# Optimization experiments

Hardware: AMD Instinct MI355X
Metric: run time of the kernel (lower is better)

The kernel has to match this reference:

```python
import jax, jax.numpy as jnp
import numpy as np

N = 4096
TAU = 0.2          # args.tau relaxation temperature
EPS = 1e-10        # numerical guard for logit of clamped probs


def setup_inputs() -> dict:
    key = jax.random.key(0)
    k1, k2, k3 = jax.random.split(key, 3)
    r = jax.random.uniform(k1, (N, N))
    ori_adj = jnp.where(r < 0.005, -1.0, jnp.where(r < 0.01, 1.0, 0.0)).astype(jnp.float32)
    # nn.init.uniform_(change_links_prob, 0.0, 0.001)
    change_links_prob = jax.random.uniform(k2, (N, N), minval=0.0, maxval=0.001, dtype=jnp.float32)
    # uniform noise for the RelaxedBernoulli logistic reparameterization
    u = jax.random.uniform(k3, (N, N), minval=1e-6, maxval=1.0 - 1e-6, dtype=jnp.float32)
    return {"ori_adj": ori_adj, "change_links_prob": change_links_prob, "u": u}


def reference(ori_adj, change_links_prob, u):
    # --- get_modified_adj: RelaxedBernoulliStraightThrough(tau, clamp(p,0,1)).rsample() ---
    p = jnp.clip(change_links_prob, EPS, 1.0 - EPS)      # torch.clamp(p, 0, 1) + logit guard
    logits = jnp.log(p) - jnp.log1p(-p)
    noise = jnp.log(u) - jnp.log1p(-u)                   # logistic noise
    soft = jax.nn.sigmoid((logits + noise) / TAU)        # relaxed sample
    hard = jnp.round(soft)                               # quantized sample
    change_prob = soft + jax.lax.stop_gradient(hard - soft)  # straight-through
    mod_adj = ori_adj + change_prob * (-2.0 * ori_adj)   # ori_adj * (1 - 2*b)

    # --- balance_degree_directed(mod_adj) ---
    # torch.diag(matrix) returns the diagonal VECTOR, broadcast-subtracted per row (faithful).
    A = mod_adj + mod_adj.T - jnp.diag(mod_adj)
    A_abs = jnp.abs(A)
    tr3 = jnp.einsum('ij,jk,ki->', A, A, A)              # trace(A @ A @ A)
    tr3_abs = jnp.einsum('ij,jk,ki->', A_abs, A_abs, A_abs)
    balance = 0.5 * (1.0 + tr3 / tr3_abs)
    return mod_adj, balance
```

## Files before the change

### kernel.cpp

```cpp
#include <hip/hip_runtime.h>
#include <hip/hip_bf16.h>
#include <cstdint>
#include <cstddef>

#define N 4096
#define NN ((size_t)N * (size_t)N)

typedef int   int4v   __attribute__((ext_vector_type(4)));
typedef float float4v __attribute__((ext_vector_type(4)));

__device__ inline void async16(const void* g, void* lds) {
    __builtin_amdgcn_global_load_lds(
        (const __attribute__((address_space(1))) void*)g,
        (__attribute__((address_space(3))) void*)lds, 16, 0, 0);
}

__global__ __launch_bounds__(256) void fused_mod_build(
        const float* __restrict__ ori,
        const float* __restrict__ clp,
        const float* __restrict__ uu,
        float* __restrict__ out,
        signed char* __restrict__ A,
        signed char* __restrict__ AT,
        signed char* __restrict__ Aa,
        signed char* __restrict__ ATa,
        double* __restrict__ accs) {
    const int I = blockIdx.x, J = blockIdx.y;
    if (I > J) return;
    __shared__ float sm1[64][65];
    __shared__ float sm2[64][65];
    __shared__ float dI[64], dJ[64];
    const int t = threadIdx.x;
    const int r = t >> 2;
    const int q = t & 3;
    const int bi = I * 64, bj = J * 64;
    if (I == 0 && J == 0 && t < 2) accs[t] = 0.0;
    if (t < 128) {
        const int x = (t < 64) ? (bi + t) : (bj + (t - 64));
        const size_t off = (size_t)x * N + x;
        const float o = ori[off];
        const float hard = (clp[off] + uu[off] >= 1.0f) ? 1.0f : 0.0f;
        const float d = fmaf(hard, -2.0f * o, o);
        if (t < 64) dI[t] = d; else dJ[t - 64] = d;
    }
    #pragma unroll
    for (int k = 0; k < 4; ++k) {
        const size_t off = (size_t)(bi + r) * N + bj + k * 16 + q * 4;
        const float4v o4 = *(const float4v*)(ori + off);
        const float4v p4 = *(const float4v*)(clp + off);
        const float4v u4 = *(const float4v*)(uu + off);
        float4v m;
        #pragma unroll
        for (int c = 0; c < 4; ++c) {
            const float hard = (p4[c] + u4[c] >= 1.0f) ? 1.0f : 0.0f;
            m[c] = fmaf(hard, -2.0f * o4[c], o4[c]);
            sm1[r][k * 16 + q * 4 + c] = m[c];
        }
        *(float4v*)(out + off) = m;
    }
    #pragma unroll
    for (int k = 0; k < 4; ++k) {
        const size_t off = (size_t)(bj + r) * N + bi + k * 16 + q * 4;
        const float4v o4 = *(const float4v*)(ori + off);
        const float4v p4 = *(const float4v*)(clp + off);
        const float4v u4 = *(const float4v*)(uu + off);
        float4v m;
        #pragma unroll
        for (int c = 0; c < 4; ++c) {
            const float hard = (p4[c] + u4[c] >= 1.0f) ? 1.0f : 0.0f;
            m[c] = fmaf(hard, -2.0f * o4[c], o4[c]);
            sm2[r][k * 16 + q * 4 + c] = m[c];
        }
        if (I != J) *(float4v*)(out + off) = m;
    }
    __syncthreads();
    int pkA1[4], pkAa1[4], pkT1[4], pkTa1[4];
    int pkA2[4], pkAa2[4], pkT2[4], pkTa2[4];
    #pragma unroll
    for (int w = 0; w < 4; ++w) {
        int a1w = 0, aa1w = 0, t1w = 0, ta1w = 0;
        int a2w = 0, aa2w = 0, t2w = 0, ta2w = 0;
        #pragma unroll
        for (int k = 0; k < 4; ++k) {
            const int c = q * 16 + w * 4 + k;
            const float a1 = sm1[r][c] + sm2[c][r] - dJ[c];
            const int v1 = (int)a1;  const int u1 = v1 < 0 ? -v1 : v1;
            a1w  |= (v1 & 255) << (8 * k);
            aa1w |= (u1 & 255) << (8 * k);
            const float t1 = sm1[c][r] + sm2[r][c] - dJ[r];
            const int w1 = (int)t1;  const int x1 = w1 < 0 ? -w1 : w1;
            t1w  |= (w1 & 255) << (8 * k);
            ta1w |= (x1 & 255) << (8 * k);
            const float a2 = sm2[r][c] + sm1[c][r] - dI[c];
            const int v2 = (int)a2;  const int u2 = v2 < 0 ? -v2 : v2;
            a2w  |= (v2 & 255) << (8 * k);
            aa2w |= (u2 & 255) << (8 * k);
            const float t2 = sm2[c][r] + sm1[r][c] - dI[r];
            const int w2 = (int)t2;  const int x2 = w2 < 0 ? -w2 : w2;
            t2w  |= (w2 & 255) << (8 * k);
            ta2w |= (x2 & 255) << (8 * k);
        }
        pkA1[w] = a1w; pkAa1[w] = aa1w; pkT1[w] = t1w; pkTa1[w] = ta1w;
        pkA2[w] = a2w; pkAa2[w] = aa2w; pkT2[w] = t2w; pkTa2[w] = ta2w;
    }
    const size_t oIJ = (size_t)(bi + r) * N + bj + q * 16;
    const size_t oJI = (size_t)(bj + r) * N + bi + q * 16;
    *(int4v*)&A  [oIJ] = *(int4v*)pkA1;
    *(int4v*)&Aa [oIJ] = *(int4v*)pkAa1;
    *(int4v*)&AT [oJI] = *(int4v*)pkT1;
    *(int4v*)&ATa[oJI] = *(int4v*)pkTa1;
    if (I != J) {
        *(int4v*)&A  [oJI] = *(int4v*)pkA2;
        *(int4v*)&Aa [oJI] = *(int4v*)pkAa2;
        *(int4v*)&AT [oIJ] = *(int4v*)pkT2;
        *(int4v*)&ATa[oIJ] = *(int4v*)pkTa2;
    }
}

#define BK 64
#define NT (N / BK)
#define BUFSZ 32768

__global__ __launch_bounds__(512, 2) void gemm_trace_i8(
        const signed char* __restrict__ Ag,
        const signed char* __restrict__ ATg,
        const signed char* __restrict__ Aag,
        const signed char* __restrict__ ATag,
        double* __restrict__ accs) {
    __shared__ __align__(16) signed char lds[4 * BUFSZ];
    __shared__ int red[8];
    const int z = blockIdx.z;
    const signed char* Asrc = z ? Aag  : Ag;
    const signed char* Bsrc = z ? ATag : ATg;
    const int i0 = blockIdx.y * 256;
    const int k0 = blockIdx.x * 256;
    const int t = threadIdx.x;
    const int lane = t & 63;
    const int wave = t >> 6;
    const int wm = wave >> 2;
    const int wn = wave & 3;
    const int quad = lane >> 4;
    const int col  = lane & 15;

    const int c1 = t;
    const int r1 = c1 >> 2;
    const int r2 = r1 + 128;
    const int s1 = (((c1 & 3) ^ ((r1 >> 1) & 3)) << 4);
    const int s2 = (((c1 & 3) ^ ((r2 >> 1) & 3)) << 4);
    const signed char* gA1 = Asrc + (size_t)(i0 + r1) * N + s1;
    const signed char* gA2 = Asrc + (size_t)(i0 + r2) * N + s2;
    const signed char* gB1 = Bsrc + (size_t)(k0 + r1) * N + s1;
    const signed char* gB2 = Bsrc + (size_t)(k0 + r2) * N + s2;
    const int ldsA1 = (wave * 64) * 16;
    const int ldsA2 = 8192  + (wave * 64) * 16;
    const int ldsB1 = 16384 + (wave * 64) * 16;
    const int ldsB2 = 24576 + (wave * 64) * 16;
    const int fsw = ((quad ^ ((col >> 1) & 3)) << 4);

    int4v acc[8][4];
    #pragma unroll
    for (int a = 0; a < 8; ++a)
        #pragma unroll
        for (int b = 0; b < 4; ++b)
            acc[a][b] = (int4v){0, 0, 0, 0};

    for (int p = 0; p < 3; ++p) {
        const int pb = p * BUFSZ;
        const size_t go = (size_t)p * BK;
        async16(gA1 + go, lds + pb + ldsA1);
        async16(gA2 + go, lds + pb + ldsA2);
        async16(gB1 + go, lds + pb + ldsB1);
        async16(gB2 + go, lds + pb + ldsB2);
    }
    asm volatile("s_waitcnt vmcnt(8)" ::: "memory");
    __builtin_amdgcn_s_barrier();
    __builtin_amdgcn_sched_barrier(0);

    for (int j = 0; j < NT; ++j) {
        const int buf = (j & 3) * BUFSZ;
        const signed char* Ab = lds + buf;
        const signed char* Bb = lds + buf + 16384;
        const int pre = j + 3;
        const size_t go = (size_t)pre * BK;
        const int pb = (pre & 3) * BUFSZ;
        int4v af0[4], af1[4], bf[4];
        af0[0] = *(const int4v*)(Ab + ((wm * 128 + 0 * 16 + col) << 6) + fsw);
        #pragma unroll
        for (int tc = 0; tc < 4; ++tc)
            bf[tc] = *(const int4v*)(Bb + ((wn * 64 + tc * 16 + col) << 6) + fsw);
        #pragma unroll
        for (int tr = 1; tr < 4; ++tr)
            af0[tr] = *(const int4v*)(Ab + ((wm * 128 + tr * 16 + col) << 6) + fsw);
        #pragma unroll
        for (int tr = 0; tr < 4; ++tr)
            af1[tr] = *(const int4v*)(Ab + ((wm * 128 + 64 + tr * 16 + col) << 6) + fsw);
        if (pre < NT) {
            async16(gA1 + go, lds + pb + ldsA1);
            async16(gA2 + go, lds + pb + ldsA2);
            async16(gB1 + go, lds + pb + ldsB1);
            async16(gB2 + go, lds + pb + ldsB2);
        }
        __builtin_amdgcn_s_setprio(1);
        asm volatile("s_waitcnt lgkmcnt(7)" ::: "memory");
        __builtin_amdgcn_sched_barrier(0);
        #pragma unroll
        for (int tc = 0; tc < 4; ++tc)
            acc[0][tc] = __builtin_amdgcn_mfma_i32_16x16x64_i8(af0[0], bf[tc], acc[0][tc], 0, 0, 0);
        #pragma unroll
        for (int tr = 1; tr < 4; ++tr) {
            if (tr == 1)      asm volatile("s_waitcnt lgkmcnt(6)" ::: "memory");
            else if (tr == 2) asm volatile("s_waitcnt lgkmcnt(5)" ::: "memory");
            else              asm volatile("s_waitcnt lgkmcnt(4)" ::: "memory");
            __builtin_amdgcn_sched_barrier(0);
            #pragma unroll
            for (int tc = 0; tc < 4; ++tc)
                acc[tr][tc] = __builtin_amdgcn_mfma_i32_16x16x64_i8(af0[tr], bf[tc], acc[tr][tc], 0, 0, 0);
        }
        #pragma unroll
        for (int tr = 0; tr < 4; ++tr) {
            if (tr == 0)      asm volatile("s_waitcnt lgkmcnt(3)" ::: "memory");
            else if (tr == 1) asm volatile("s_waitcnt lgkmcnt(2)" ::: "memory");
            else if (tr == 2) asm volatile("s_waitcnt lgkmcnt(1)" ::: "memory");
            else              asm volatile("s_waitcnt lgkmcnt(0)" ::: "memory");
            __builtin_amdgcn_sched_barrier(0);
            #pragma unroll
            for (int tc = 0; tc < 4; ++tc)
                acc[4 + tr][tc] = __builtin_amdgcn_mfma_i32_16x16x64_i8(af1[tr], bf[tc], acc[4 + tr][tc], 0, 0, 0);
        }
        __builtin_amdgcn_s_setprio(0);
        if (j < NT - 3)       { asm volatile("s_waitcnt vmcnt(8)" ::: "memory"); }
        else if (j == NT - 3) { asm volatile("s_waitcnt vmcnt(4)" ::: "memory"); }
        else if (j == NT - 2) { asm volatile("s_waitcnt vmcnt(0)" ::: "memory"); }
        __builtin_amdgcn_s_barrier();
        __builtin_amdgcn_sched_barrier(0);
    }

    int part = 0;
    #pragma unroll
    for (int mr = 0; mr < 8; ++mr) {
        const int ib = i0 + wm * 128 + mr * 16 + quad * 4;
        #pragma unroll
        for (int tc = 0; tc < 4; ++tc) {
            const int kk = k0 + wn * 64 + tc * 16 + col;
            const int mv = *(const int*)&Asrc[(size_t)kk * N + ib];
            #pragma unroll
            for (int r = 0; r < 4; ++r)
                part += acc[mr][tc][r] * (int)(signed char)(mv >> (8 * r));
        }
    }
    #pragma unroll
    for (int off = 32; off > 0; off >>= 1)
        part += __shfl_down(part, off, 64);
    if (lane == 0) red[wave] = part;
    __syncthreads();
    if (t == 0) {
        int tot = 0;
        #pragma unroll
        for (int w = 0; w < 8; ++w) tot += red[w];
        atomicAdd(&accs[z], (double)tot);
    }
}

__global__ void finalize_kernel(const double* __restrict__ accs, float* __restrict__ out) {
    out[NN] = (float)(0.5 * (1.0 + accs[0] / accs[1]));
}

extern "C" void kernel_launch(void* const* d_in, const int* in_sizes, int n_in,
                              void* d_out, int out_size, void* d_ws, size_t ws_size,
                              hipStream_t stream) {
    const float* ori = (const float*)d_in[0];
    const float* clp = (const float*)d_in[1];
    const float* u   = (const float*)d_in[2];
    float* out = (float*)d_out;
    char* ws = (char*)d_ws;
    signed char* A8   = (signed char*)ws;
    signed char* AT8  = (signed char*)(ws + NN);
    signed char* Aa8  = (signed char*)(ws + 2 * NN);
    signed char* ATa8 = (signed char*)(ws + 3 * NN);
    double*      accs = (double*)(ws + 4 * NN);

    fused_mod_build<<<dim3(64, 64), 256, 0, stream>>>(
        ori, clp, u, out, A8, AT8, Aa8, ATa8, accs);
    gemm_trace_i8<<<dim3(N / 256, N / 256, 2), 512, 0, stream>>>(A8, AT8, Aa8, ATa8, accs);
    finalize_kernel<<<1, 1, 0, stream>>>(accs, out);
}
```

Measured before the change: 386.3 us.

## Split build tiles across two thread halves and coarsen GEMM LDS waits

The build kernel now launches 512 threads per tile pair, and each half loads, transforms and packs one of the two mirrored 64x64 tiles. Previously each thread did both, so this doubles thread-level parallelism and halves per-thread register pressure. In the int8 GEMM loop, the per-row fine-grained lgkmcnt waits are replaced by two coarse waits, one before each half of the MFMA block, with the priority toggled around each. That cuts wait/barrier instructions but can expose more LDS latency before the first MFMAs.

After: 393.7 us. About the same (+1.9%).

```diff
diff --git a/kernel.cpp b/kernel.cpp
--- a/kernel.cpp
+++ b/kernel.cpp
@@ -15,7 +15,7 @@
         (__attribute__((address_space(3))) void*)lds, 16, 0, 0);
 }
 
-__global__ __launch_bounds__(256) void fused_mod_build(
+__global__ __launch_bounds__(512) void fused_mod_build(
         const float* __restrict__ ori,
         const float* __restrict__ clp,
         const float* __restrict__ uu,
@@ -30,9 +30,11 @@
     __shared__ float sm1[64][65];
     __shared__ float sm2[64][65];
     __shared__ float dI[64], dJ[64];
-    const int t = threadIdx.x;
-    const int r = t >> 2;
-    const int q = t & 3;
+    const int t    = threadIdx.x;
+    const int half = t >> 8;
+    const int tt   = t & 255;
+    const int r    = tt >> 2;
+    const int q    = tt & 3;
     const int bi = I * 64, bj = J * 64;
     if (I == 0 && J == 0 && t < 2) accs[t] = 0.0;
     if (t < 128) {
@@ -43,73 +45,74 @@
         const float d = fmaf(hard, -2.0f * o, o);
         if (t < 64) dI[t] = d; else dJ[t - 64] = d;
     }
-    #pragma unroll
-    for (int k = 0; k < 4; ++k) {
-        const size_t off = (size_t)(bi + r) * N + bj + k * 16 + q * 4;
-        const float4v o4 = *(const float4v*)(ori + off);
-        const float4v p4 = *(const float4v*)(clp + off);
-        const float4v u4 = *(const float4v*)(uu + off);
-        float4v m;
-        #pragma unroll
-        for (int c = 0; c < 4; ++c) {
-            const float hard = (p4[c] + u4[c] >= 1.0f) ? 1.0f : 0.0f;
-            m[c] = fmaf(hard, -2.0f * o4[c], o4[c]);
-            sm1[r][k * 16 + q * 4 + c] = m[c];
-        }
-        *(float4v*)(out + off) = m;
-    }
-    #pragma unroll
-    for (int k = 0; k < 4; ++k) {
-        const size_t off = (size_t)(bj + r) * N + bi + k * 16 + q * 4;
-        const float4v o4 = *(const float4v*)(ori + off);
-        const float4v p4 = *(const float4v*)(clp + off);
-        const float4v u4 = *(const float4v*)(uu + off);
-        float4v m;
-        #pragma unroll
-        for (int c = 0; c < 4; ++c) {
-            const float hard = (p4[c] + u4[c] >= 1.0f) ? 1.0f : 0.0f;
-            m[c] = fmaf(hard, -2.0f * o4[c], o4[c]);
-            sm2[r][k * 16 + q * 4 + c] = m[c];
-        }
-        if (I != J) *(float4v*)(out + off) = m;
+    {
+        const int rowbase = half ? bj : bi;
+        const int colbase = half ? bi : bj;
+        float (*sm)[65] = half ? sm2 : sm1;
+        const bool wr = (half == 0) || (I != J);
+        #pragma unroll
+        for (int k = 0; k < 4; ++k) {
+            const size_t off = (size_t)(rowbase + r) * N + colbase + k * 16 + q * 4;
+            const float4v o4 = *(const float4v*)(ori + off);
+            const float4v p4 = *(const float4v*)(clp + off);
+            const float4v u4 = *(const float4v*)(uu + off);
+            float4v m;
+            #pragma unroll
+            for (int c = 0; c < 4; ++c) {
+                const float hard = (p4[c] + u4[c] >= 1.0f) ? 1.0f : 0.0f;
+                m[c] = fmaf(hard, -2.0f * o4[c], o4[c]);
+                sm[r][k * 16 + q * 4 + c] = m[c];
+            }
+            if (wr) *(float4v*)(out + off) = m;
+        }
     }
     __syncthreads();
-    int pkA1[4], pkAa1[4], pkT1[4], pkTa1[4];
-    int pkA2[4], pkAa2[4], pkT2[4], pkTa2[4];
-    #pragma unroll
-    for (int w = 0; w < 4; ++w) {
-        int a1w = 0, aa1w = 0, t1w = 0, ta1w = 0;
-        int a2w = 0, aa2w = 0, t2w = 0, ta2w = 0;
-        #pragma unroll
-        for (int k = 0; k < 4; ++k) {
-            const int c = q * 16 + w * 4 + k;
-            const float a1 = sm1[r][c] + sm2[c][r] - dJ[c];
-            const int v1 = (int)a1;  const int u1 = v1 < 0 ? -v1 : v1;
-            a1w  |= (v1 & 255) << (8 * k);
-            aa1w |= (u1 & 255) << (8 * k);
-            const float t1 = sm1[c][r] + sm2[r][c] - dJ[r];
-            const int w1 = (int)t1;  const int x1 = w1 < 0 ? -w1 : w1;
-            t1w  |= (w1 & 255) << (8 * k);
-            ta1w |= (x1 & 255) << (8 * k);
-            const float a2 = sm2[r][c] + sm1[c][r] - dI[c];
-            const int v2 = (int)a2;  const int u2 = v2 < 0 ? -v2 : v2;
-            a2w  |= (v2 & 255) << (8 * k);
-            aa2w |= (u2 & 255) << (8 * k);
-            const float t2 = sm2[c][r] + sm1[r][c] - dI[r];
-            const int w2 = (int)t2;  const int x2 = w2 < 0 ? -w2 : w2;
-            t2w  |= (w2 & 255) << (8 * k);
-            ta2w |= (x2 & 255) << (8 * k);
-        }
-        pkA1[w] = a1w; pkAa1[w] = aa1w; pkT1[w] = t1w; pkTa1[w] = ta1w;
-        pkA2[w] = a2w; pkAa2[w] = aa2w; pkT2[w] = t2w; pkTa2[w] = ta2w;
-    }
-    const size_t oIJ = (size_t)(bi + r) * N + bj + q * 16;
-    const size_t oJI = (size_t)(bj + r) * N + bi + q * 16;
-    *(int4v*)&A  [oIJ] = *(int4v*)pkA1;
-    *(int4v*)&Aa [oIJ] = *(int4v*)pkAa1;
-    *(int4v*)&AT [oJI] = *(int4v*)pkT1;
-    *(int4v*)&ATa[oJI] = *(int4v*)pkTa1;
-    if (I != J) {
+    if (half == 0) {
+        int pkA1[4], pkAa1[4], pkT1[4], pkTa1[4];
+        #pragma unroll
+        for (int w = 0; w < 4; ++w) {
+            int a1w = 0, aa1w = 0, t1w = 0, ta1w = 0;
+            #pragma unroll
+            for (int k = 0; k < 4; ++k) {
+                const int c = q * 16 + w * 4 + k;
+                const float a1 = sm1[r][c] + sm2[c][r] - dJ[c];
+                const int v1 = (int)a1;  const int u1 = v1 < 0 ? -v1 : v1;
+                a1w  |= (v1 & 255) << (8 * k);
+                aa1w |= (u1 & 255) << (8 * k);
+                const float t1 = sm1[c][r] + sm2[r][c] - dJ[r];
+                const int w1 = (int)t1;  const int x1 = w1 < 0 ? -w1 : w1;
+                t1w  |= (w1 & 255) << (8 * k);
+                ta1w |= (x1 & 255) << (8 * k);
+            }
+            pkA1[w] = a1w; pkAa1[w] = aa1w; pkT1[w] = t1w; pkTa1[w] = ta1w;
+        }
+        const size_t oIJ = (size_t)(bi + r) * N + bj + q * 16;
+        const size_t oJI = (size_t)(bj + r) * N + bi + q * 16;
+        *(int4v*)&A  [oIJ] = *(int4v*)pkA1;
+        *(int4v*)&Aa [oIJ] = *(int4v*)pkAa1;
+        *(int4v*)&AT [oJI] = *(int4v*)pkT1;
+        *(int4v*)&ATa[oJI] = *(int4v*)pkTa1;
+    } else if (I != J) {
+        int pkA2[4], pkAa2[4], pkT2[4], pkTa2[4];
+        #pragma unroll
+        for (int w = 0; w < 4; ++w) {
+            int a2w = 0, aa2w = 0, t2w = 0, ta2w = 0;
+            #pragma unroll
+            for (int k = 0; k < 4; ++k) {
+                const int c = q * 16 + w * 4 + k;
+                const float a2 = sm2[r][c] + sm1[c][r] - dI[c];
+                const int v2 = (int)a2;  const int u2 = v2 < 0 ? -v2 : v2;
+                a2w  |= (v2 & 255) << (8 * k);
+                aa2w |= (u2 & 255) << (8 * k);
+                const float t2 = sm2[c][r] + sm1[r][c] - dI[r];
+                const int w2 = (int)t2;  const int x2 = w2 < 0 ? -w2 : w2;
+                t2w  |= (w2 & 255) << (8 * k);
+                ta2w |= (x2 & 255) << (8 * k);
+            }
+            pkA2[w] = a2w; pkAa2[w] = aa2w; pkT2[w] = t2w; pkTa2[w] = ta2w;
+        }
+        const size_t oIJ = (size_t)(bi + r) * N + bj + q * 16;
+        const size_t oJI = (size_t)(bj + r) * N + bi + q * 16;
         *(int4v*)&A  [oJI] = *(int4v*)pkA2;
         *(int4v*)&Aa [oJI] = *(int4v*)pkAa2;
         *(int4v*)&AT [oIJ] = *(int4v*)pkT2;
@@ -184,13 +187,12 @@
         const size_t go = (size_t)pre * BK;
         const int pb = (pre & 3) * BUFSZ;
         int4v af0[4], af1[4], bf[4];
-        af0[0] = *(const int4v*)(Ab + ((wm * 128 + 0 * 16 + col) << 6) + fsw);
+        #pragma unroll
+        for (int tr = 0; tr < 4; ++tr)
+            af0[tr] = *(const int4v*)(Ab + ((wm * 128 + tr * 16 + col) << 6) + fsw);
         #pragma unroll
         for (int tc = 0; tc < 4; ++tc)
             bf[tc] = *(const int4v*)(Bb + ((wn * 64 + tc * 16 + col) << 6) + fsw);
-        #pragma unroll
-        for (int tr = 1; tr < 4; ++tr)
-            af0[tr] = *(const int4v*)(Ab + ((wm * 128 + tr * 16 + col) << 6) + fsw);
         #pragma unroll
         for (int tr = 0; tr < 4; ++tr)
             af1[tr] = *(const int4v*)(Ab + ((wm * 128 + 64 + tr * 16 + col) << 6) + fsw);
@@ -200,33 +202,23 @@
             async16(gB1 + go, lds + pb + ldsB1);
             async16(gB2 + go, lds + pb + ldsB2);
         }
+        asm volatile("s_waitcnt lgkmcnt(4)" ::: "memory");
+        __builtin_amdgcn_sched_barrier(0);
         __builtin_amdgcn_s_setprio(1);
-        asm volatile("s_waitcnt lgkmcnt(7)" ::: "memory");
-        __builtin_amdgcn_sched_barrier(0);
-        #pragma unroll
-        for (int tc = 0; tc < 4; ++tc)
-            acc[0][tc] = __builtin_amdgcn_mfma_i32_16x16x64_i8(af0[0], bf[tc], acc[0][tc], 0, 0, 0);
-        #pragma unroll
-        for (int tr = 1; tr < 4; ++tr) {
-            if (tr == 1)      asm volatile("s_waitcnt lgkmcnt(6)" ::: "memory");
-            else if (tr == 2) asm volatile("s_waitcnt lgkmcnt(5)" ::: "memory");
-            else              asm volatile("s_waitcnt lgkmcnt(4)" ::: "memory");
-            __builtin_amdgcn_sched_barrier(0);
+        #pragma unroll
+        for (int tr = 0; tr < 4; ++tr)
             #pragma unroll
             for (int tc = 0; tc < 4; ++tc)
                 acc[tr][tc] = __builtin_amdgcn_mfma_i32_16x16x64_i8(af0[tr], bf[tc], acc[tr][tc], 0, 0, 0);
-        }
-        #pragma unroll
-        for (int tr = 0; tr < 4; ++tr) {
-            if (tr == 0)      asm volatile("s_waitcnt lgkmcnt(3)" ::: "memory");
-            else if (tr == 1) asm volatile("s_waitcnt lgkmcnt(2)" ::: "memory");
-            else if (tr == 2) asm volatile("s_waitcnt lgkmcnt(1)" ::: "memory");
-            else              asm volatile("s_waitcnt lgkmcnt(0)" ::: "memory");
-            __builtin_amdgcn_sched_barrier(0);
+        __builtin_amdgcn_s_setprio(0);
+        asm volatile("s_waitcnt lgkmcnt(0)" ::: "memory");
+        __builtin_amdgcn_sched_barrier(0);
+        __builtin_amdgcn_s_setprio(1);
+        #pragma unroll
+        for (int tr = 0; tr < 4; ++tr)
             #pragma unroll
             for (int tc = 0; tc < 4; ++tc)
                 acc[4 + tr][tc] = __builtin_amdgcn_mfma_i32_16x16x64_i8(af1[tr], bf[tc], acc[4 + tr][tc], 0, 0, 0);
-        }
         __builtin_amdgcn_s_setprio(0);
         if (j < NT - 3)       { asm volatile("s_waitcnt vmcnt(8)" ::: "memory"); }
         else if (j == NT - 3) { asm volatile("s_waitcnt vmcnt(4)" ::: "memory"); }
@@ -279,7 +271,7 @@
     signed char* ATa8 = (signed char*)(ws + 3 * NN);
     double*      accs = (double*)(ws + 4 * NN);
 
-    fused_mod_build<<<dim3(64, 64), 256, 0, stream>>>(
+    fused_mod_build<<<dim3(64, 64), 512, 0, stream>>>(
         ori, clp, u, out, A8, AT8, Aa8, ATa8, accs);
     gemm_trace_i8<<<dim3(N / 256, N / 256, 2), 512, 0, stream>>>(A8, AT8, Aa8, ATa8, accs);
     finalize_kernel<<<1, 1, 0, stream>>>(accs, out);
```
